# Optimization experiments

Measured on AMD Instinct MI355X. Metric: run time of the kernel, lower is better.

Reference implementation:

```python
import jax, jax.numpy as jnp
import numpy as np

EPS = 1e-8
Q_MAX = 127.0  # 2**(8-1) - 1


def _activation_quant(x):
    gamma = jnp.maximum(jnp.max(jnp.abs(x)), EPS)
    scale = Q_MAX / gamma
    x_int = jnp.clip(jnp.round(x * scale), -Q_MAX, Q_MAX)
    x_fq = x_int / scale
    # straight-through estimator
    return x + jax.lax.stop_gradient(x_fq - x)


def _weight_quant(w):
    gamma = jnp.maximum(jnp.mean(jnp.abs(w)), EPS)
    w_int = jnp.clip(jnp.round(w / gamma), -1.0, 1.0)
    w_fq = w_int * gamma
    return w + jax.lax.stop_gradient(w_fq - w)


def setup_inputs() -> dict:
    key = jax.random.key(0)
    kx, kw, kb = jax.random.split(key, 3)
    in_features, out_features = 2048, 2048
    x = jax.random.normal(kx, (4, 4096, in_features), dtype=jnp.float32)
    # nn.Linear default init: U(-1/sqrt(fan_in), 1/sqrt(fan_in))
    bound = 1.0 / np.sqrt(in_features)
    W = jax.random.uniform(kw, (out_features, in_features), dtype=jnp.float32,
                           minval=-bound, maxval=bound)
    b = jax.random.uniform(kb, (out_features,), dtype=jnp.float32,
                           minval=-bound, maxval=bound)
    return {"x": x, "W": W, "b": b}


def reference(x, W, b):
    x_q = _activation_quant(x)          # int8 absmax fake-quant
    w_q = _weight_quant(W)              # ternary {-g, 0, g} fake-quant
    # F.linear: x @ W^T + b
    return jnp.einsum('bsi,oi->bso', x_q, w_q) + b
```

## Files before the change

### kernel.cpp

```cpp
#include <hip/hip_runtime.h>
#include <hip/hip_bf16.h>
#include <stdint.h>

typedef __attribute__((ext_vector_type(4))) int i32x4;

static constexpr long M_ = 16384;
static constexpr long N_ = 2048;
static constexpr long K_ = 2048;

#define BM 128
#define BN 128
#define BKB 64

#define GLOAD_LDS16(g, l)                                                          \
  __builtin_amdgcn_global_load_lds(                                               \
      (const __attribute__((address_space(1))) unsigned int*)(g),                 \
      (__attribute__((address_space(3))) unsigned int*)(l), 16, 0, 0)

__global__ __launch_bounds__(64) void k_init(double* gw_sum, unsigned* gx_bits) {
  if (threadIdx.x == 0) {
    *gw_sum = 0.0;
    *gx_bits = 0u;
  }
}

__global__ __launch_bounds__(256) void k_absmax(const float4* __restrict__ x, long n4,
                                                unsigned* __restrict__ gx_bits) {
  float m = 0.0f;
  const long stride = (long)gridDim.x * blockDim.x;
  for (long i = (long)blockIdx.x * blockDim.x + threadIdx.x; i < n4; i += stride) {
    float4 v = x[i];
    m = fmaxf(m, fmaxf(fmaxf(fabsf(v.x), fabsf(v.y)), fmaxf(fabsf(v.z), fabsf(v.w))));
  }
#pragma unroll
  for (int off = 32; off > 0; off >>= 1) m = fmaxf(m, __shfl_down(m, off));
  __shared__ float sm[4];
  const int lane = threadIdx.x & 63, wv = threadIdx.x >> 6;
  if (lane == 0) sm[wv] = m;
  __syncthreads();
  if (threadIdx.x == 0) {
    float bm = fmaxf(fmaxf(sm[0], sm[1]), fmaxf(sm[2], sm[3]));
    atomicMax(gx_bits, __float_as_uint(bm));
  }
}

__global__ __launch_bounds__(256) void k_abssum(const float4* __restrict__ w, long n4,
                                                double* __restrict__ gw_sum) {
  double s = 0.0;
  const long stride = (long)gridDim.x * blockDim.x;
  for (long i = (long)blockIdx.x * blockDim.x + threadIdx.x; i < n4; i += stride) {
    float4 v = w[i];
    s += (double)fabsf(v.x) + (double)fabsf(v.y) + (double)fabsf(v.z) + (double)fabsf(v.w);
  }
#pragma unroll
  for (int off = 32; off > 0; off >>= 1) s += __shfl_down(s, off);
  __shared__ double sd[4];
  const int lane = threadIdx.x & 63, wv = threadIdx.x >> 6;
  if (lane == 0) sd[wv] = s;
  __syncthreads();
  if (threadIdx.x == 0) atomicAdd(gw_sum, (sd[0] + sd[1]) + (sd[2] + sd[3]));
}

__global__ __launch_bounds__(256) void k_quant_x(const float4* __restrict__ x,
                                                 char4* __restrict__ xq, long n4,
                                                 const unsigned* __restrict__ gx_bits) {
  const double gx = (double)fmaxf(__uint_as_float(*gx_bits), 1e-8f);
  const double scale = 127.0 / gx;
  const long stride = (long)gridDim.x * blockDim.x;
  for (long i = (long)blockIdx.x * blockDim.x + threadIdx.x; i < n4; i += stride) {
    float4 v = x[i];
    char4 o;
    o.x = (signed char)(int)fmin(fmax(rint((double)v.x * scale), -127.0), 127.0);
    o.y = (signed char)(int)fmin(fmax(rint((double)v.y * scale), -127.0), 127.0);
    o.z = (signed char)(int)fmin(fmax(rint((double)v.z * scale), -127.0), 127.0);
    o.w = (signed char)(int)fmin(fmax(rint((double)v.w * scale), -127.0), 127.0);
    xq[i] = o;
  }
}

__global__ __launch_bounds__(256) void k_quant_w(const float4* __restrict__ w,
                                                 char4* __restrict__ wq, long n4,
                                                 const double* __restrict__ gw_sum) {
  const double gw = fmax(*gw_sum * (1.0 / 4194304.0), 1e-8);
  const long stride = (long)gridDim.x * blockDim.x;
  for (long i = (long)blockIdx.x * blockDim.x + threadIdx.x; i < n4; i += stride) {
    float4 v = w[i];
    char4 o;
    o.x = (signed char)(int)fmin(fmax(rint((double)v.x / gw), -1.0), 1.0);
    o.y = (signed char)(int)fmin(fmax(rint((double)v.y / gw), -1.0), 1.0);
    o.z = (signed char)(int)fmin(fmax(rint((double)v.z / gw), -1.0), 1.0);
    o.w = (signed char)(int)fmin(fmax(rint((double)v.w / gw), -1.0), 1.0);
    wq[i] = o;
  }
}

__global__ __launch_bounds__(256, 2) void k_gemm(
    const signed char* __restrict__ Aq, const signed char* __restrict__ Bq,
    const float* __restrict__ bias, float* __restrict__ out,
    const unsigned* __restrict__ gx_bits, const double* __restrict__ gw_sum) {
  __shared__ signed char As[BM * BKB];
  __shared__ signed char Bs[BN * BKB];

  const int tid = threadIdx.x;
  const int lane = tid & 63;
  const int wv = tid >> 6;
  const int wr = wv >> 1;
  const int wc = wv & 1;

  const int wg = (int)((blockIdx.x & 7) * 256 + (blockIdx.x >> 3));
  const int nblocks_n = (int)(N_ / BN);
  const int nblk = wg % nblocks_n;
  const int mblk = wg / nblocks_n;
  const long brow = (long)mblk * BM;
  const long bcol = (long)nblk * BN;

  i32x4 acc[4][4];
#pragma unroll
  for (int m = 0; m < 4; m++)
#pragma unroll
    for (int n = 0; n < 4; n++) acc[m][n] = (i32x4){0, 0, 0, 0};

  const int ch0 = tid;
  const int ch1 = tid + 256;
  const signed char* A0 = Aq + (brow + (ch0 >> 2)) * K_ + (ch0 & 3) * 16;
  const signed char* A1 = Aq + (brow + (ch1 >> 2)) * K_ + (ch1 & 3) * 16;
  const signed char* B0 = Bq + (bcol + (ch0 >> 2)) * K_ + (ch0 & 3) * 16;
  const signed char* B1 = Bq + (bcol + (ch1 >> 2)) * K_ + (ch1 & 3) * 16;
  signed char* lA0 = &As[ch0 * 16];
  signed char* lA1 = &As[ch1 * 16];
  signed char* lB0 = &Bs[ch0 * 16];
  signed char* lB1 = &Bs[ch1 * 16];

  const int koff = (lane >> 4) * 16;
  const int rsel = lane & 15;

  for (int kt = 0; kt < (int)K_; kt += BKB) {
    GLOAD_LDS16(A0 + kt, lA0);
    GLOAD_LDS16(A1 + kt, lA1);
    GLOAD_LDS16(B0 + kt, lB0);
    GLOAD_LDS16(B1 + kt, lB1);
    __syncthreads();

    i32x4 a[4], b[4];
#pragma unroll
    for (int m = 0; m < 4; m++)
      a[m] = *(const i32x4*)(&As[(wr * 64 + m * 16 + rsel) * BKB + koff]);
#pragma unroll
    for (int n = 0; n < 4; n++)
      b[n] = *(const i32x4*)(&Bs[(wc * 64 + n * 16 + rsel) * BKB + koff]);

#pragma unroll
    for (int m = 0; m < 4; m++)
#pragma unroll
      for (int n = 0; n < 4; n++)
        acc[m][n] = __builtin_amdgcn_mfma_i32_16x16x64_i8(a[m], b[n], acc[m][n], 0, 0, 0);
    __syncthreads();
  }

  const float gxf = fmaxf(__uint_as_float(*gx_bits), 1e-8f);
  const double gwd = fmax(*gw_sum * (1.0 / 4194304.0), 1e-8);
  const float alpha = (float)((double)gxf * gwd * (1.0 / 127.0));

#pragma unroll
  for (int n = 0; n < 4; n++) {
    const long col = bcol + wc * 64 + n * 16 + (lane & 15);
    const float bv = bias[col];
#pragma unroll
    for (int m = 0; m < 4; m++) {
      const long row0 = brow + wr * 64 + m * 16 + (lane >> 4) * 4;
#pragma unroll
      for (int r = 0; r < 4; r++) {
        out[(row0 + r) * N_ + col] = (float)acc[m][n][r] * alpha + bv;
      }
    }
  }
}

extern "C" void kernel_launch(void* const* d_in, const int* in_sizes, int n_in,
                              void* d_out, int out_size, void* d_ws, size_t ws_size,
                              hipStream_t stream) {
  const float* x = (const float*)d_in[0];
  const float* W = (const float*)d_in[1];
  const float* b = (const float*)d_in[2];
  float* out = (float*)d_out;

  char* ws = (char*)d_ws;
  double* gw_sum = (double*)ws;
  unsigned* gx_bits = (unsigned*)(ws + 8);
  signed char* xq = (signed char*)(ws + 256);
  signed char* wq = (signed char*)(ws + 256 + (size_t)M_ * (size_t)K_);

  const long nx4 = M_ * K_ / 4;
  const long nw4 = N_ * K_ / 4;

  hipLaunchKernelGGL(k_init, dim3(1), dim3(64), 0, stream, gw_sum, gx_bits);
  hipLaunchKernelGGL(k_absmax, dim3(2048), dim3(256), 0, stream,
                     (const float4*)x, nx4, gx_bits);
  hipLaunchKernelGGL(k_abssum, dim3(512), dim3(256), 0, stream,
                     (const float4*)W, nw4, gw_sum);
  hipLaunchKernelGGL(k_quant_x, dim3(2048), dim3(256), 0, stream,
                     (const float4*)x, (char4*)xq, nx4, gx_bits);
  hipLaunchKernelGGL(k_quant_w, dim3(512), dim3(256), 0, stream,
                     (const float4*)W, (char4*)wq, nw4, gw_sum);
  hipLaunchKernelGGL(k_gemm, dim3((unsigned)((M_ / BM) * (N_ / BN))), dim3(256), 0, stream,
                     xq, wq, b, out, gx_bits, gw_sum);
}
```

Before: 180.2 us.

## Rewrite int8 GEMM as 256x256 tile with multi-stage swizzled LDS pipeline

Measured after the change: 171.0 us. 5.1% less time.

```diff
diff --git a/kernel.cpp b/kernel.cpp
--- a/kernel.cpp
+++ b/kernel.cpp
@@ -8,9 +8,6 @@
 static constexpr long N_ = 2048;
 static constexpr long K_ = 2048;
 
-#define BM 128
-#define BN 128
-#define BKB 64
 
 #define GLOAD_LDS16(g, l)                                                          \
   __builtin_amdgcn_global_load_lds(                                               \
@@ -94,67 +91,107 @@
   }
 }
 
-__global__ __launch_bounds__(256, 2) void k_gemm(
+
+__device__ __forceinline__ void stageq(signed char* lds, const signed char* gp,
+                                       int isb, int buf, int ks, int kbase, int tid) {
+  signed char* lr = lds + isb * 65536 + buf * 32768 + ks * 16384;
+  const int w = tid >> 6, lane = tid & 63;
+#pragma unroll
+  for (int s = 0; s < 2; ++s) {
+    const int slot = w * 2 + s;
+    const int r = slot * 16 + (lane >> 2);
+    const int c = (lane & 3) ^ ((r >> 1) & 3);
+    GLOAD_LDS16(gp + (long)r * K_ + kbase + c * 16, lr + slot * 1024);
+  }
+}
+
+__device__ __forceinline__ i32x4 lds_frag(const signed char* region, int row, int lane) {
+  const int swz = (((lane >> 4) ^ ((row >> 1) & 3)) << 4);
+  return *(const i32x4*)(region + row * 64 + swz);
+}
+
+template <int BUF, int KS, int MH, int SGB, int SGBUF, int SGKS, int VM>
+__device__ __forceinline__ void phase(signed char* lds, const signed char* Ap,
+                                      const signed char* Bp, int sg_kbase, int wave_m,
+                                      int wave_n, int lane, int tid,
+                                      i32x4 acc[8][4], i32x4 b4[4]) {
+  const signed char* Ar = lds + BUF * 32768 + KS * 16384;
+  const signed char* Br = lds + 65536 + BUF * 32768 + KS * 16384;
+  i32x4 a4[4];
+  if (MH == 0) {
+#pragma unroll
+    for (int n = 0; n < 4; ++n)
+      b4[n] = lds_frag(Br, wave_n * 64 + n * 16 + (lane & 15), lane);
+  }
+#pragma unroll
+  for (int mm = 0; mm < 4; ++mm)
+    a4[mm] = lds_frag(Ar, wave_m * 128 + MH * 64 + mm * 16 + (lane & 15), lane);
+
+  stageq(lds, SGB ? Bp : Ap, SGB, SGBUF, SGKS, sg_kbase, tid);
+
+  __builtin_amdgcn_s_barrier();
+  asm volatile("s_waitcnt lgkmcnt(0)" ::: "memory");
+  __builtin_amdgcn_s_setprio(1);
+#pragma unroll
+  for (int mm = 0; mm < 4; ++mm)
+#pragma unroll
+    for (int n = 0; n < 4; ++n)
+      acc[MH * 4 + mm][n] =
+          __builtin_amdgcn_mfma_i32_16x16x64_i8(a4[mm], b4[n], acc[MH * 4 + mm][n], 0, 0, 0);
+  __builtin_amdgcn_s_setprio(0);
+  if (VM) asm volatile("s_waitcnt vmcnt(8)" ::: "memory");
+  __builtin_amdgcn_s_barrier();
+}
+
+__global__ __launch_bounds__(512, 2) void k_gemm(
     const signed char* __restrict__ Aq, const signed char* __restrict__ Bq,
     const float* __restrict__ bias, float* __restrict__ out,
     const unsigned* __restrict__ gx_bits, const double* __restrict__ gw_sum) {
-  __shared__ signed char As[BM * BKB];
-  __shared__ signed char Bs[BN * BKB];
+  extern __shared__ signed char lds[];
 
   const int tid = threadIdx.x;
   const int lane = tid & 63;
-  const int wv = tid >> 6;
-  const int wr = wv >> 1;
-  const int wc = wv & 1;
-
-  const int wg = (int)((blockIdx.x & 7) * 256 + (blockIdx.x >> 3));
-  const int nblocks_n = (int)(N_ / BN);
-  const int nblk = wg % nblocks_n;
-  const int mblk = wg / nblocks_n;
-  const long brow = (long)mblk * BM;
-  const long bcol = (long)nblk * BN;
-
-  i32x4 acc[4][4];
-#pragma unroll
-  for (int m = 0; m < 4; m++)
+  const int wid = tid >> 6;
+  const int wave_m = wid >> 2;
+  const int wave_n = wid & 3;
+
+  const int wg = (int)((blockIdx.x & 7) * 64 + (blockIdx.x >> 3));
+  const int nblk = wg & 7;
+  const int mblk = wg >> 3;
+  const long brow = (long)mblk * 256;
+  const long bcol = (long)nblk * 256;
+
+  const signed char* Ap = Aq + brow * K_;
+  const signed char* Bp = Bq + bcol * K_;
+
+  i32x4 acc[8][4];
+#pragma unroll
+  for (int m = 0; m < 8; m++)
 #pragma unroll
     for (int n = 0; n < 4; n++) acc[m][n] = (i32x4){0, 0, 0, 0};
-
-  const int ch0 = tid;
-  const int ch1 = tid + 256;
-  const signed char* A0 = Aq + (brow + (ch0 >> 2)) * K_ + (ch0 & 3) * 16;
-  const signed char* A1 = Aq + (brow + (ch1 >> 2)) * K_ + (ch1 & 3) * 16;
-  const signed char* B0 = Bq + (bcol + (ch0 >> 2)) * K_ + (ch0 & 3) * 16;
-  const signed char* B1 = Bq + (bcol + (ch1 >> 2)) * K_ + (ch1 & 3) * 16;
-  signed char* lA0 = &As[ch0 * 16];
-  signed char* lA1 = &As[ch1 * 16];
-  signed char* lB0 = &Bs[ch0 * 16];
-  signed char* lB1 = &Bs[ch1 * 16];
-
-  const int koff = (lane >> 4) * 16;
-  const int rsel = lane & 15;
-
-  for (int kt = 0; kt < (int)K_; kt += BKB) {
-    GLOAD_LDS16(A0 + kt, lA0);
-    GLOAD_LDS16(A1 + kt, lA1);
-    GLOAD_LDS16(B0 + kt, lB0);
-    GLOAD_LDS16(B1 + kt, lB1);
-    __syncthreads();
-
-    i32x4 a[4], b[4];
-#pragma unroll
-    for (int m = 0; m < 4; m++)
-      a[m] = *(const i32x4*)(&As[(wr * 64 + m * 16 + rsel) * BKB + koff]);
-#pragma unroll
-    for (int n = 0; n < 4; n++)
-      b[n] = *(const i32x4*)(&Bs[(wc * 64 + n * 16 + rsel) * BKB + koff]);
-
-#pragma unroll
-    for (int m = 0; m < 4; m++)
-#pragma unroll
-      for (int n = 0; n < 4; n++)
-        acc[m][n] = __builtin_amdgcn_mfma_i32_16x16x64_i8(a[m], b[n], acc[m][n], 0, 0, 0);
-    __syncthreads();
+  i32x4 b4[4];
+
+  stageq(lds, Ap, 0, 0, 0, 0, tid);
+  stageq(lds, Bp, 1, 0, 0, 0, tid);
+  stageq(lds, Ap, 0, 0, 1, 64, tid);
+  stageq(lds, Bp, 1, 0, 1, 64, tid);
+  stageq(lds, Ap, 0, 1, 0, 128, tid);
+  stageq(lds, Bp, 1, 1, 0, 128, tid);
+  asm volatile("s_waitcnt vmcnt(0)" ::: "memory");
+  __builtin_amdgcn_s_barrier();
+
+  for (int kt = 0; kt < (int)K_; kt += 256) {
+    const int k1 = (kt + 128) & 2047;
+    const int k2 = (kt + 256) & 2047;
+    const int k3 = (kt + 384) & 2047;
+    phase<0, 0, 0, 0, 1, 1, 0>(lds, Ap, Bp, k1 + 64, wave_m, wave_n, lane, tid, acc, b4);
+    phase<0, 0, 1, 1, 1, 1, 1>(lds, Ap, Bp, k1 + 64, wave_m, wave_n, lane, tid, acc, b4);
+    phase<0, 1, 0, 0, 0, 0, 0>(lds, Ap, Bp, k2, wave_m, wave_n, lane, tid, acc, b4);
+    phase<0, 1, 1, 1, 0, 0, 1>(lds, Ap, Bp, k2, wave_m, wave_n, lane, tid, acc, b4);
+    phase<1, 0, 0, 0, 0, 1, 0>(lds, Ap, Bp, k2 + 64, wave_m, wave_n, lane, tid, acc, b4);
+    phase<1, 0, 1, 1, 0, 1, 1>(lds, Ap, Bp, k2 + 64, wave_m, wave_n, lane, tid, acc, b4);
+    phase<1, 1, 0, 0, 1, 0, 0>(lds, Ap, Bp, k3, wave_m, wave_n, lane, tid, acc, b4);
+    phase<1, 1, 1, 1, 1, 0, 1>(lds, Ap, Bp, k3, wave_m, wave_n, lane, tid, acc, b4);
   }
 
   const float gxf = fmaxf(__uint_as_float(*gx_bits), 1e-8f);
@@ -162,14 +199,14 @@
   const float alpha = (float)((double)gxf * gwd * (1.0 / 127.0));
 
 #pragma unroll
-  for (int n = 0; n < 4; n++) {
-    const long col = bcol + wc * 64 + n * 16 + (lane & 15);
+  for (int n = 0; n < 4; ++n) {
+    const long col = bcol + wave_n * 64 + n * 16 + (lane & 15);
     const float bv = bias[col];
 #pragma unroll
-    for (int m = 0; m < 4; m++) {
-      const long row0 = brow + wr * 64 + m * 16 + (lane >> 4) * 4;
-#pragma unroll
-      for (int r = 0; r < 4; r++) {
+    for (int m = 0; m < 8; ++m) {
+      const long row0 = brow + wave_m * 128 + m * 16 + (lane >> 4) * 4;
+#pragma unroll
+      for (int r = 0; r < 4; ++r) {
         out[(row0 + r) * N_ + col] = (float)acc[m][n][r] * alpha + bv;
       }
     }
@@ -192,6 +229,13 @@
 
   const long nx4 = M_ * K_ / 4;
   const long nw4 = N_ * K_ / 4;
+
+  static bool attr_set = false;
+  if (!attr_set) {
+    (void)hipFuncSetAttribute(reinterpret_cast<const void*>(&k_gemm),
+                              hipFuncAttributeMaxDynamicSharedMemorySize, 131072);
+    attr_set = true;
+  }
 
   hipLaunchKernelGGL(k_init, dim3(1), dim3(64), 0, stream, gw_sum, gx_bits);
   hipLaunchKernelGGL(k_absmax, dim3(2048), dim3(256), 0, stream,
@@ -202,6 +246,6 @@
                      (const float4*)x, (char4*)xq, nx4, gx_bits);
   hipLaunchKernelGGL(k_quant_w, dim3(512), dim3(256), 0, stream,
                      (const float4*)W, (char4*)wq, nw4, gw_sum);
-  hipLaunchKernelGGL(k_gemm, dim3((unsigned)((M_ / BM) * (N_ / BN))), dim3(256), 0, stream,
-                     xq, wq, b, out, gx_bits, gw_sum);
-}
+  hipLaunchKernelGGL(k_gemm, dim3((unsigned)((M_ / 256) * (N_ / 256))), dim3(512),
+                     131072, stream, xq, wq, b, out, gx_bits, gw_sum);
+}
```
